# Optimization experiments

Measured on AMD Instinct MI355X. Metric: run time of the kernel, lower is better.

Reference implementation:

```python
import jax, jax.numpy as jnp
import numpy as np

N_NODES = 50000
N_EDGES = 500000


def setup_inputs() -> dict:
    key = jax.random.key(0)
    ks = jax.random.split(key, 24)
    p = {}
    p['x_feat'] = jax.random.normal(ks[0], (N_NODES, 24), dtype=jnp.float32)
    p['edge_index'] = jax.random.randint(ks[1], (2, N_EDGES), 0, N_NODES)
    p['edge_attr'] = jax.random.uniform(ks[2], (N_EDGES, 16), dtype=jnp.float32)
    def lin(k, fan_in, shape):
        b = 1.0 / np.sqrt(fan_in)
        return jax.random.uniform(k, shape, jnp.float32, -b, b)
    # group-0 input projection: 24 -> 32
    p['lin_prep_W'] = lin(ks[3], 24, (24, 32)); p['lin_prep_b'] = lin(ks[4], 24, (32,))
    # prep tube: 32 -> 16
    p['tube_W'] = lin(ks[5], 32, (32, 16)); p['tube_b'] = lin(ks[6], 32, (16,))
    # shared edge-attr trunk: 16 -> 32 -> 16
    p['edge_W1'] = lin(ks[7], 16, (16, 32)); p['edge_b1'] = lin(ks[8], 16, (32,))
    p['edge_W2'] = lin(ks[9], 32, (32, 16)); p['edge_b2'] = lin(ks[10], 32, (16,))
    # conv1: in=16, out=8 per aggr (mean, max, add)
    p['conv1_edge_W'] = lin(ks[11], 16, (3, 16, 16 * 8)); p['conv1_edge_b'] = lin(ks[12], 16, (3, 16 * 8))
    p['conv1_root_W'] = lin(ks[13], 16, (3, 16, 8)); p['conv1_bias'] = lin(ks[14], 16, (3, 8))
    # conv2: in=24, out=8 per aggr
    p['conv2_edge_W'] = lin(ks[15], 16, (3, 16, 24 * 8)); p['conv2_edge_b'] = lin(ks[16], 16, (3, 24 * 8))
    p['conv2_root_W'] = lin(ks[17], 24, (3, 24, 8)); p['conv2_bias'] = lin(ks[18], 24, (3, 8))
    # output head: 24 -> 2
    p['out_W'] = lin(ks[19], 24, (24, 2)); p['out_b'] = lin(ks[20], 24, (2,))
    return p


def _nnconv(x, e_repr, src, dst, edge_W, edge_b, root_W, bias, n_nodes):
    # x: [N, in]; e_repr: [E, 16]; edge_W: [3, 16, in*out]
    d_in = x.shape[1]
    x_src = x[src]  # [E, in]
    deg = jax.ops.segment_sum(jnp.ones_like(src, dtype=x.dtype), dst, num_segments=n_nodes)  # [N]
    outs = []
    for a, aggr in enumerate(('mean', 'max', 'add')):
        W_e = (e_repr @ edge_W[a] + edge_b[a]).reshape(e_repr.shape[0], d_in, -1)  # [E, in, out]
        msg = jnp.einsum('ei,eio->eo', x_src, W_e)  # [E, out]
        if aggr == 'add':
            agg = jax.ops.segment_sum(msg, dst, num_segments=n_nodes)
        elif aggr == 'mean':
            agg = jax.ops.segment_sum(msg, dst, num_segments=n_nodes) / jnp.maximum(deg, 1.0)[:, None]
        else:
            agg = jax.ops.segment_max(msg, dst, num_segments=n_nodes)
            agg = jnp.where(deg[:, None] > 0, agg, 0.0)  # no-neighbor nodes -> 0
        outs.append(agg + x @ root_W[a] + bias[a])
    return jax.nn.relu(jnp.concatenate(outs, axis=1))  # [N, 3*out]


def reference(x_feat, edge_index, edge_attr, lin_prep_W, lin_prep_b, tube_W, tube_b,
              edge_W1, edge_b1, edge_W2, edge_b2,
              conv1_edge_W, conv1_edge_b, conv1_root_W, conv1_bias,
              conv2_edge_W, conv2_edge_b, conv2_root_W, conv2_bias,
              out_W, out_b):
    n_nodes = x_feat.shape[0]
    src, dst = edge_index[0], edge_index[1]
    # node prep: group projection + tube (relu acts, dropout=0 -> identity)
    x = jax.nn.relu(x_feat @ lin_prep_W + lin_prep_b)       # [N, 32]
    x = jax.nn.relu(x @ tube_W + tube_b)                    # [N, 16]
    # shared edge-attr trunk (last activation = sigmoid), computed once
    e = jax.nn.relu(edge_attr @ edge_W1 + edge_b1)
    e_repr = jax.nn.sigmoid(e @ edge_W2 + edge_b2)          # [E, 16]
    # hop 1 and hop 2 of edge-conditioned NNConv with mean/max/add aggregators
    x = _nnconv(x, e_repr, src, dst, conv1_edge_W, conv1_edge_b, conv1_root_W, conv1_bias, n_nodes)  # [N, 24]
    x = _nnconv(x, e_repr, src, dst, conv2_edge_W, conv2_edge_b, conv2_root_W, conv2_bias, n_nodes)  # [N, 24]
    logits = x @ out_W + out_b                              # [N, 2]
    scores = jax.nn.softmax(logits, axis=1)
    return (logits, scores)
```

## Files before the change

kernel.cpp:

```cpp
#include <hip/hip_runtime.h>

#define BS 256

__device__ __forceinline__ unsigned short f2bf(float f) {
    unsigned x = __float_as_uint(f);
    return (unsigned short)((x + 0x7fffu + ((x >> 16) & 1u)) >> 16);
}
__device__ __forceinline__ void unpack8(uint4 v, float* d) {
    d[0] = __uint_as_float(v.x << 16); d[1] = __uint_as_float(v.x & 0xFFFF0000u);
    d[2] = __uint_as_float(v.y << 16); d[3] = __uint_as_float(v.y & 0xFFFF0000u);
    d[4] = __uint_as_float(v.z << 16); d[5] = __uint_as_float(v.z & 0xFFFF0000u);
    d[6] = __uint_as_float(v.w << 16); d[7] = __uint_as_float(v.w & 0xFFFF0000u);
}
__device__ __forceinline__ uint4 pack8bf(const float* r) {
    unsigned w[4];
#pragma unroll
    for (int j = 0; j < 4; j++)
        w[j] = (unsigned)f2bf(r[2 * j]) | ((unsigned)f2bf(r[2 * j + 1]) << 16);
    return make_uint4(w[0], w[1], w[2], w[3]);
}
__device__ __forceinline__ void st24bf(unsigned short* p, const float* r) {
    uint4* q = (uint4*)p;
    q[0] = pack8bf(r);
    q[1] = pack8bf(r + 8);
    q[2] = pack8bf(r + 16);
}

__global__ void prep_kernel(const float* __restrict__ xf,
                            const float* __restrict__ W1, const float* __restrict__ b1,
                            const float* __restrict__ W2, const float* __restrict__ b2,
                            float* __restrict__ x16, int N)
{
    int n = blockIdx.x * blockDim.x + threadIdx.x;
    bool valid = n < N;
    int nn = valid ? n : 0;
    float a[24];
#pragma unroll
    for (int i = 0; i < 24; i += 4)
        *(float4*)(a + i) = *(const float4*)(xf + (size_t)nn * 24 + i);
    float h[32];
#pragma unroll
    for (int j = 0; j < 32; j++) {
        float s = b1[j];
#pragma unroll
        for (int i = 0; i < 24; i++) s = fmaf(a[i], W1[i * 32 + j], s);
        h[j] = fmaxf(s, 0.f);
    }
    if (!valid) return;
#pragma unroll
    for (int j = 0; j < 16; j++) {
        float s = b2[j];
#pragma unroll
        for (int i = 0; i < 32; i++) s = fmaf(h[i], W2[i * 16 + j], s);
        x16[(size_t)n * 16 + j] = fmaxf(s, 0.f);
    }
}

__global__ void degjj_kernel(const int* __restrict__ srcA, const int* __restrict__ dstA,
                             int* __restrict__ cntS, int* __restrict__ cntD,
                             int* __restrict__ jS, int* __restrict__ jD, int E)
{
    int e = blockIdx.x * blockDim.x + threadIdx.x;
    if (e < E) {
        jS[e] = atomicAdd(&cntS[srcA[e]], 1);
        jD[e] = atomicAdd(&cntD[dstA[e]], 1);
    }
}
__global__ void offsets2_kernel(const int* __restrict__ cntS, const int* __restrict__ cntD,
                                int* __restrict__ offsS, int* __restrict__ offsD,
                                int* __restrict__ cursS, int* __restrict__ cursD, int N)
{
    int n = blockIdx.x * blockDim.x + threadIdx.x;
    int lane = threadIdx.x & 63;
    bool valid = n < N;
    int dS = valid ? cntS[n] : 0;
    int dD = valid ? cntD[n] : 0;
    int sS = dS, sD = dD;
#pragma unroll
    for (int o = 1; o < 64; o <<= 1) {
        int tS = __shfl_up(sS, o);
        int tD = __shfl_up(sD, o);
        if (lane >= o) { sS += tS; sD += tD; }
    }
    int totS = __shfl(sS, 63);
    int totD = __shfl(sD, 63);
    int baseS = 0, baseD = 0;
    if (lane == 63) {
        baseS = atomicAdd(cursS, totS);
        baseD = atomicAdd(cursD, totD);
    }
    baseS = __shfl(baseS, 63);
    baseD = __shfl(baseD, 63);
    if (valid) {
        offsS[n] = baseS + sS - dS;
        offsD[n] = baseD + sD - dD;
    }
}

__global__ __launch_bounds__(BS) void er_fill_kernel(
    const int* __restrict__ srcA, const int* __restrict__ dstA,
    const int* __restrict__ jS, const int* __restrict__ jD,
    const int* __restrict__ offsS, const int* __restrict__ offsD,
    const float* __restrict__ eattr,
    const float* __restrict__ eW1, const float* __restrict__ eb1,
    const float* __restrict__ eW2, const float* __restrict__ eb2,
    uint2* __restrict__ spq, unsigned short* __restrict__ er_s, int E)
{
    int e = blockIdx.x * BS + threadIdx.x;
    if (e >= E) return;
    int s = srcA[e], d = dstA[e];
    int p = offsS[s] + jS[e];
    int q = offsD[d] + jD[e];
    spq[p] = make_uint2((unsigned)s, (unsigned)q);

    float ea[16];
#pragma unroll
    for (int i = 0; i < 16; i += 4)
        *(float4*)(ea + i) = *(const float4*)(eattr + (size_t)e * 16 + i);
    float h[32];
#pragma unroll
    for (int j = 0; j < 32; j++) {
        float t = eb1[j];
#pragma unroll
        for (int i = 0; i < 16; i++) t = fmaf(ea[i], eW1[i * 32 + j], t);
        h[j] = fmaxf(t, 0.f);
    }
    float er[16];
#pragma unroll
    for (int j = 0; j < 16; j++) {
        float t = eb2[j];
#pragma unroll
        for (int i = 0; i < 32; i++) t = fmaf(h[i], eW2[i * 16 + j], t);
        er[j] = 1.f / (1.f + __expf(-t));
    }
    uint4* qo = (uint4*)(er_s + (size_t)p * 16);
    qo[0] = pack8bf(er);
    qo[1] = pack8bf(er + 8);
}

template <int IN>
__global__ __launch_bounds__(BS) void ynode_kernel(const float* __restrict__ x,
                                                   const float* __restrict__ W,
                                                   const float* __restrict__ B,
                                                   const float* __restrict__ RW,
                                                   const float* __restrict__ RB,
                                                   unsigned short* __restrict__ Y,
                                                   float* __restrict__ root, int N)
{
    __shared__ float w_lds[IN * 24];
    int t = threadIdx.x;
    int k = blockIdx.y;

    for (int idx = t; idx < IN * 24; idx += BS) {
        int i = idx / 24;
        int j = idx - i * 24;
        int a = j >> 3, o = j & 7;
        float v;
        if (k < 16)       v = W[(((size_t)a * 16 + k) * IN + i) * 8 + o];
        else if (k == 16) v = B[((size_t)a * IN + i) * 8 + o];
        else              v = RW[((size_t)a * IN + i) * 8 + o];
        w_lds[idx] = v;
    }
    __syncthreads();

    int n0 = blockIdx.x * (BS * 2) + t;
    int n1 = n0 + BS;
    bool v0 = n0 < N, v1 = n1 < N;
    int m0 = v0 ? n0 : 0, m1 = v1 ? n1 : 0;

    float xa[IN], xb[IN];
#pragma unroll
    for (int i = 0; i < IN; i += 4) {
        *(float4*)(xa + i) = *(const float4*)(x + (size_t)m0 * IN + i);
        *(float4*)(xb + i) = *(const float4*)(x + (size_t)m1 * IN + i);
    }

    float ra[24], rb[24];
    if (k == 17) {
#pragma unroll
        for (int j = 0; j < 24; j++) { ra[j] = RB[j]; rb[j] = ra[j]; }
    } else {
#pragma unroll
        for (int j = 0; j < 24; j++) { ra[j] = 0.f; rb[j] = 0.f; }
    }

#pragma unroll
    for (int i = 0; i < IN; i++) {
        float x0 = xa[i], x1 = xb[i];
        const float* wr = w_lds + i * 24;
#pragma unroll
        for (int j = 0; j < 24; j++) {
            float w = wr[j];
            ra[j] = fmaf(x0, w, ra[j]);
            rb[j] = fmaf(x1, w, rb[j]);
        }
    }

    if (k < 17) {
        if (v0) st24bf(Y + ((size_t)k * N + n0) * 24, ra);
        if (v1) st24bf(Y + ((size_t)k * N + n1) * 24, rb);
    } else {
        if (v0) {
            float* pr = root + (size_t)n0 * 24;
#pragma unroll
            for (int j = 0; j < 24; j += 4)
                *(float4*)(pr + j) = make_float4(ra[j], ra[j+1], ra[j+2], ra[j+3]);
        }
        if (v1) {
            float* pr = root + (size_t)n1 * 24;
#pragma unroll
            for (int j = 0; j < 24; j += 4)
                *(float4*)(pr + j) = make_float4(rb[j], rb[j+1], rb[j+2], rb[j+3]);
        }
    }
}

__global__ __launch_bounds__(BS) void msg_kernel(
    const uint2* __restrict__ spq,
    const unsigned short* __restrict__ er_s,
    const unsigned short* __restrict__ Y,
    unsigned short* __restrict__ msg16,
    int N, int E)
{
    int tid = blockIdx.x * BS + threadIdx.x;
    int p = tid / 3;
    int j = tid - p * 3;
    if (p >= E) return;

    uint2 sq = spq[p];

    float er[16];
    {
        const uint4* eu = (const uint4*)(er_s + (size_t)p * 16);
        unpack8(eu[0], er);
        unpack8(eu[1], er + 8);
    }

    const unsigned short* yb = Y + (size_t)sq.x * 24 + j * 8;
    size_t kstride = (size_t)N * 24;

    float acc[8];
    unpack8(*(const uint4*)(yb + 16 * kstride), acc);
#pragma unroll
    for (int k = 0; k < 16; k++) {
        float t[8];
        unpack8(*(const uint4*)(yb + (size_t)k * kstride), t);
        float ek = er[k];
#pragma unroll
        for (int o = 0; o < 8; o++) acc[o] = fmaf(ek, t[o], acc[o]);
    }
    unsigned short* mrow = msg16 + (size_t)sq.y * 32;
    *(uint4*)(mrow + j * 8) = pack8bf(acc);
    if (j == 0) *(uint4*)(mrow + 24) = make_uint4(0, 0, 0, 0);
}

__global__ __launch_bounds__(BS) void gather_kernel(
    const unsigned short* __restrict__ msg16,
    const int* __restrict__ offs,
    const int* __restrict__ degi,
    const float* __restrict__ root,
    float* __restrict__ out, int N)
{
    int n = (blockIdx.x * BS + threadIdx.x) >> 6;
    if (n >= N) return;
    int lane = threadIdx.x & 63;
    int c = lane & 3;
    int r = lane >> 2;

    int off = offs[n];
    int d = degi[n];

    float s[8], m[8];
#pragma unroll
    for (int o = 0; o < 8; o++) { s[o] = 0.f; m[o] = -3.402823466e38f; }

    if (c < 3) {
        const unsigned short* base = msg16 + (size_t)off * 32 + c * 8;
        for (int j = r; j < d; j += 16) {
            uint4 v = *(const uint4*)(base + (size_t)j * 32);
            float t[8];
            unpack8(v, t);
#pragma unroll
            for (int o = 0; o < 8; o++) {
                s[o] += t[o];
                m[o] = fmaxf(m[o], t[o]);
            }
        }
    }
#pragma unroll
    for (int mask = 4; mask < 64; mask <<= 1) {
#pragma unroll
        for (int o = 0; o < 8; o++) {
            s[o] += __shfl_xor(s[o], mask);
            m[o] = fmaxf(m[o], __shfl_xor(m[o], mask));
        }
    }
    if (lane >= 3) return;

    float inv = 1.f / fmaxf((float)d, 1.f);
    const float* pr = root + (size_t)n * 24 + c * 8;
    float4 r0 = *(const float4*)(pr);
    float4 r1 = *(const float4*)(pr + 4);
    float rb[8] = {r0.x, r0.y, r0.z, r0.w, r1.x, r1.y, r1.z, r1.w};
    float rr[8];
#pragma unroll
    for (int o = 0; o < 8; o++) {
        float agg = (c == 0) ? s[o] * inv
                  : (c == 1) ? ((d > 0) ? m[o] : 0.f)
                  : s[o];
        rr[o] = fmaxf(rb[o] + agg, 0.f);
    }
    float* po = out + (size_t)n * 24 + c * 8;
    *(float4*)(po)     = make_float4(rr[0], rr[1], rr[2], rr[3]);
    *(float4*)(po + 4) = make_float4(rr[4], rr[5], rr[6], rr[7]);
}

__global__ void head_kernel(const float* __restrict__ x, const float* __restrict__ W,
                            const float* __restrict__ b, float* __restrict__ out, int N)
{
    int n = blockIdx.x * blockDim.x + threadIdx.x;
    if (n >= N) return;
    float l0 = b[0], l1 = b[1];
#pragma unroll
    for (int i = 0; i < 24; i++) {
        float xi = x[(size_t)n * 24 + i];
        l0 = fmaf(xi, W[i * 2 + 0], l0);
        l1 = fmaf(xi, W[i * 2 + 1], l1);
    }
    out[2 * (size_t)n + 0] = l0;
    out[2 * (size_t)n + 1] = l1;
    float mx = fmaxf(l0, l1);
    float e0 = __expf(l0 - mx), e1 = __expf(l1 - mx);
    float sm = e0 + e1;
    out[2 * (size_t)N + 2 * (size_t)n + 0] = e0 / sm;
    out[2 * (size_t)N + 2 * (size_t)n + 1] = e1 / sm;
}

extern "C" void kernel_launch(void* const* d_in, const int* in_sizes, int n_in,
                              void* d_out, int out_size, void* d_ws, size_t ws_size,
                              hipStream_t stream)
{
    const float* x_feat = (const float*)d_in[0];
    const int*   eidx   = (const int*)d_in[1];
    const float* eattr  = (const float*)d_in[2];
    const float* lpW = (const float*)d_in[3];
    const float* lpb = (const float*)d_in[4];
    const float* tW  = (const float*)d_in[5];
    const float* tb  = (const float*)d_in[6];
    const float* eW1 = (const float*)d_in[7];
    const float* eb1 = (const float*)d_in[8];
    const float* eW2 = (const float*)d_in[9];
    const float* eb2 = (const float*)d_in[10];
    const float* c1W = (const float*)d_in[11];
    const float* c1B = (const float*)d_in[12];
    const float* c1R = (const float*)d_in[13];
    const float* c1b = (const float*)d_in[14];
    const float* c2W = (const float*)d_in[15];
    const float* c2B = (const float*)d_in[16];
    const float* c2R = (const float*)d_in[17];
    const float* c2b = (const float*)d_in[18];
    const float* oW  = (const float*)d_in[19];
    const float* ob  = (const float*)d_in[20];

    int N = in_sizes[0] / 24;
    int E = in_sizes[1] / 2;
    const int* srcA = eidx;
    const int* dstA = eidx + E;

    char* wsb = (char*)d_ws;
    size_t off = 0;
    auto alloc = [&](size_t bytes) {
        off = (off + 255) & ~(size_t)255;
        void* p = wsb + off;
        off += bytes;
        return p;
    };
    unsigned short* Y     = (unsigned short*)alloc((size_t)17 * N * 24 * 2);
    unsigned short* msg16 = (unsigned short*)alloc((size_t)E * 32 * 2);
    unsigned short* er_s  = (unsigned short*)alloc((size_t)E * 16 * 2);
    float* root = (float*)alloc((size_t)N * 24 * 4);
    float* x16  = (float*)alloc((size_t)N * 16 * 4);
    float* x24a = (float*)alloc((size_t)N * 24 * 4);
    float* x24b = (float*)alloc((size_t)N * 24 * 4);
    int* ibase  = (int*)alloc(((size_t)2 * N + 2) * 4);
    int* cntS = ibase;
    int* cntD = ibase + N;
    int* cursS = ibase + 2 * N;
    int* cursD = ibase + 2 * N + 1;
    int* offsS = (int*)alloc((size_t)N * 4);
    int* offsD = (int*)alloc((size_t)N * 4);
    int* jS    = (int*)alloc((size_t)E * 4);
    int* jD    = (int*)alloc((size_t)E * 4);
    uint2* spq = (uint2*)alloc((size_t)E * 8);

    dim3 blk(BS);
    int nb_nodes = (N + BS - 1) / BS;
    int nb_edges = (E + BS - 1) / BS;
    int nb_msg   = (3 * E + BS - 1) / BS;
    int nb_gath  = ((size_t)N * 64 + BS - 1) / BS;
    int nb_ypair = (N + BS * 2 - 1) / (BS * 2);
    dim3 ygrid(nb_ypair, 18);

    hipMemsetAsync(ibase, 0, (2 * (size_t)N + 2) * 4, stream);

    prep_kernel<<<nb_nodes, blk, 0, stream>>>(x_feat, lpW, lpb, tW, tb, x16, N);

    degjj_kernel<<<nb_edges, blk, 0, stream>>>(srcA, dstA, cntS, cntD, jS, jD, E);
    offsets2_kernel<<<nb_nodes, blk, 0, stream>>>(cntS, cntD, offsS, offsD, cursS, cursD, N);
    er_fill_kernel<<<nb_edges, blk, 0, stream>>>(srcA, dstA, jS, jD, offsS, offsD,
                                                 eattr, eW1, eb1, eW2, eb2, spq, er_s, E);

    ynode_kernel<16><<<ygrid, blk, 0, stream>>>(x16, c1W, c1B, c1R, c1b, Y, root, N);
    msg_kernel<<<nb_msg, blk, 0, stream>>>(spq, er_s, Y, msg16, N, E);
    gather_kernel<<<nb_gath, blk, 0, stream>>>(msg16, offsD, cntD, root, x24a, N);

    ynode_kernel<24><<<ygrid, blk, 0, stream>>>(x24a, c2W, c2B, c2R, c2b, Y, root, N);
    msg_kernel<<<nb_msg, blk, 0, stream>>>(spq, er_s, Y, msg16, N, E);
    gather_kernel<<<nb_gath, blk, 0, stream>>>(msg16, offsD, cntD, root, x24b, N);

    head_kernel<<<nb_nodes, blk, 0, stream>>>(x24b, oW, ob, (float*)d_out, N);
}
```

Measured before the change: 276.3 us.

## Split Y and root into per-aggregator planes and batch degree atomics per thread

```diff
diff --git a/kernel.cpp b/kernel.cpp
--- a/kernel.cpp
+++ b/kernel.cpp
@@ -19,12 +19,6 @@
         w[j] = (unsigned)f2bf(r[2 * j]) | ((unsigned)f2bf(r[2 * j + 1]) << 16);
     return make_uint4(w[0], w[1], w[2], w[3]);
 }
-__device__ __forceinline__ void st24bf(unsigned short* p, const float* r) {
-    uint4* q = (uint4*)p;
-    q[0] = pack8bf(r);
-    q[1] = pack8bf(r + 8);
-    q[2] = pack8bf(r + 16);
-}
 
 __global__ void prep_kernel(const float* __restrict__ xf,
                             const float* __restrict__ W1, const float* __restrict__ b1,
@@ -60,12 +54,25 @@
                              int* __restrict__ cntS, int* __restrict__ cntD,
                              int* __restrict__ jS, int* __restrict__ jD, int E)
 {
-    int e = blockIdx.x * blockDim.x + threadIdx.x;
-    if (e < E) {
-        jS[e] = atomicAdd(&cntS[srcA[e]], 1);
-        jD[e] = atomicAdd(&cntD[dstA[e]], 1);
-    }
-}
+    int base = blockIdx.x * (BS * 4) + threadIdx.x;
+    int e0 = base, e1 = base + BS, e2 = base + 2 * BS, e3 = base + 3 * BS;
+    bool v0 = e0 < E, v1 = e1 < E, v2 = e2 < E, v3 = e3 < E;
+    int s0 = 0, s1 = 0, s2 = 0, s3 = 0, d0 = 0, d1 = 0, d2 = 0, d3 = 0;
+    if (v0) { s0 = srcA[e0]; d0 = dstA[e0]; }
+    if (v1) { s1 = srcA[e1]; d1 = dstA[e1]; }
+    if (v2) { s2 = srcA[e2]; d2 = dstA[e2]; }
+    if (v3) { s3 = srcA[e3]; d3 = dstA[e3]; }
+    int a0 = 0, a1 = 0, a2 = 0, a3 = 0, b0 = 0, b1 = 0, b2 = 0, b3 = 0;
+    if (v0) { a0 = atomicAdd(&cntS[s0], 1); b0 = atomicAdd(&cntD[d0], 1); }
+    if (v1) { a1 = atomicAdd(&cntS[s1], 1); b1 = atomicAdd(&cntD[d1], 1); }
+    if (v2) { a2 = atomicAdd(&cntS[s2], 1); b2 = atomicAdd(&cntD[d2], 1); }
+    if (v3) { a3 = atomicAdd(&cntS[s3], 1); b3 = atomicAdd(&cntD[d3], 1); }
+    if (v0) { jS[e0] = a0; jD[e0] = b0; }
+    if (v1) { jS[e1] = a1; jD[e1] = b1; }
+    if (v2) { jS[e2] = a2; jD[e2] = b2; }
+    if (v3) { jS[e3] = a3; jD[e3] = b3; }
+}
+
 __global__ void offsets2_kernel(const int* __restrict__ cntS, const int* __restrict__ cntD,
                                 int* __restrict__ offsS, int* __restrict__ offsD,
                                 int* __restrict__ cursS, int* __restrict__ cursD, int N)
@@ -147,20 +154,16 @@
                                                    unsigned short* __restrict__ Y,
                                                    float* __restrict__ root, int N)
 {
-    __shared__ float w_lds[IN * 24];
+    __shared__ float4 w4[IN * 2];
     int t = threadIdx.x;
     int k = blockIdx.y;
-
-    for (int idx = t; idx < IN * 24; idx += BS) {
-        int i = idx / 24;
-        int j = idx - i * 24;
-        int a = j >> 3, o = j & 7;
-        float v;
-        if (k < 16)       v = W[(((size_t)a * 16 + k) * IN + i) * 8 + o];
-        else if (k == 16) v = B[((size_t)a * IN + i) * 8 + o];
-        else              v = RW[((size_t)a * IN + i) * 8 + o];
-        w_lds[idx] = v;
-    }
+    int a = blockIdx.z;
+
+    const float* wbase;
+    if (k < 16)       wbase = W + (((size_t)a * 16 + k) * IN) * 8;
+    else if (k == 16) wbase = B + ((size_t)a * IN) * 8;
+    else              wbase = RW + ((size_t)a * IN) * 8;
+    if (t < IN * 2) w4[t] = ((const float4*)wbase)[t];
     __syncthreads();
 
     int n0 = blockIdx.x * (BS * 2) + t;
@@ -175,42 +178,41 @@
         *(float4*)(xb + i) = *(const float4*)(x + (size_t)m1 * IN + i);
     }
 
-    float ra[24], rb[24];
-    if (k == 17) {
-#pragma unroll
-        for (int j = 0; j < 24; j++) { ra[j] = RB[j]; rb[j] = ra[j]; }
+    float r0[8], r1[8];
+#pragma unroll
+    for (int o = 0; o < 8; o++) { r0[o] = 0.f; r1[o] = 0.f; }
+
+#pragma unroll
+    for (int i = 0; i < IN; i++) {
+        float4 wA = w4[i * 2];
+        float4 wB = w4[i * 2 + 1];
+        float x0 = xa[i], x1 = xb[i];
+        r0[0] = fmaf(x0, wA.x, r0[0]); r0[1] = fmaf(x0, wA.y, r0[1]);
+        r0[2] = fmaf(x0, wA.z, r0[2]); r0[3] = fmaf(x0, wA.w, r0[3]);
+        r0[4] = fmaf(x0, wB.x, r0[4]); r0[5] = fmaf(x0, wB.y, r0[5]);
+        r0[6] = fmaf(x0, wB.z, r0[6]); r0[7] = fmaf(x0, wB.w, r0[7]);
+        r1[0] = fmaf(x1, wA.x, r1[0]); r1[1] = fmaf(x1, wA.y, r1[1]);
+        r1[2] = fmaf(x1, wA.z, r1[2]); r1[3] = fmaf(x1, wA.w, r1[3]);
+        r1[4] = fmaf(x1, wB.x, r1[4]); r1[5] = fmaf(x1, wB.y, r1[5]);
+        r1[6] = fmaf(x1, wB.z, r1[6]); r1[7] = fmaf(x1, wB.w, r1[7]);
+    }
+
+    if (k < 17) {
+        size_t slab = ((size_t)k * 3 + a) * N;
+        if (v0) *(uint4*)(Y + (slab + n0) * 8) = pack8bf(r0);
+        if (v1) *(uint4*)(Y + (slab + n1) * 8) = pack8bf(r1);
     } else {
-#pragma unroll
-        for (int j = 0; j < 24; j++) { ra[j] = 0.f; rb[j] = 0.f; }
-    }
-
-#pragma unroll
-    for (int i = 0; i < IN; i++) {
-        float x0 = xa[i], x1 = xb[i];
-        const float* wr = w_lds + i * 24;
-#pragma unroll
-        for (int j = 0; j < 24; j++) {
-            float w = wr[j];
-            ra[j] = fmaf(x0, w, ra[j]);
-            rb[j] = fmaf(x1, w, rb[j]);
-        }
-    }
-
-    if (k < 17) {
-        if (v0) st24bf(Y + ((size_t)k * N + n0) * 24, ra);
-        if (v1) st24bf(Y + ((size_t)k * N + n1) * 24, rb);
-    } else {
+        float rb0 = RB[a * 8 + 0], rb1 = RB[a * 8 + 1], rb2 = RB[a * 8 + 2], rb3 = RB[a * 8 + 3];
+        float rb4 = RB[a * 8 + 4], rb5 = RB[a * 8 + 5], rb6 = RB[a * 8 + 6], rb7 = RB[a * 8 + 7];
         if (v0) {
-            float* pr = root + (size_t)n0 * 24;
-#pragma unroll
-            for (int j = 0; j < 24; j += 4)
-                *(float4*)(pr + j) = make_float4(ra[j], ra[j+1], ra[j+2], ra[j+3]);
+            float* pr = root + ((size_t)a * N + n0) * 8;
+            *(float4*)(pr)     = make_float4(r0[0] + rb0, r0[1] + rb1, r0[2] + rb2, r0[3] + rb3);
+            *(float4*)(pr + 4) = make_float4(r0[4] + rb4, r0[5] + rb5, r0[6] + rb6, r0[7] + rb7);
         }
         if (v1) {
-            float* pr = root + (size_t)n1 * 24;
-#pragma unroll
-            for (int j = 0; j < 24; j += 4)
-                *(float4*)(pr + j) = make_float4(rb[j], rb[j+1], rb[j+2], rb[j+3]);
+            float* pr = root + ((size_t)a * N + n1) * 8;
+            *(float4*)(pr)     = make_float4(r1[0] + rb0, r1[1] + rb1, r1[2] + rb2, r1[3] + rb3);
+            *(float4*)(pr + 4) = make_float4(r1[4] + rb4, r1[5] + rb5, r1[6] + rb6, r1[7] + rb7);
         }
     }
 }
@@ -236,8 +238,8 @@
         unpack8(eu[1], er + 8);
     }
 
-    const unsigned short* yb = Y + (size_t)sq.x * 24 + j * 8;
-    size_t kstride = (size_t)N * 24;
+    const unsigned short* yb = Y + ((size_t)j * N + sq.x) * 8;
+    size_t kstride = (size_t)3 * N * 8;
 
     float acc[8];
     unpack8(*(const uint4*)(yb + 16 * kstride), acc);
@@ -298,7 +300,7 @@
     if (lane >= 3) return;
 
     float inv = 1.f / fmaxf((float)d, 1.f);
-    const float* pr = root + (size_t)n * 24 + c * 8;
+    const float* pr = root + ((size_t)c * N + n) * 8;
     float4 r0 = *(const float4*)(pr);
     float4 r1 = *(const float4*)(pr + 4);
     float rb[8] = {r0.x, r0.y, r0.z, r0.w, r1.x, r1.y, r1.z, r1.w};
@@ -375,10 +377,10 @@
         off += bytes;
         return p;
     };
-    unsigned short* Y     = (unsigned short*)alloc((size_t)17 * N * 24 * 2);
+    unsigned short* Y     = (unsigned short*)alloc((size_t)17 * 3 * N * 8 * 2);
     unsigned short* msg16 = (unsigned short*)alloc((size_t)E * 32 * 2);
     unsigned short* er_s  = (unsigned short*)alloc((size_t)E * 16 * 2);
-    float* root = (float*)alloc((size_t)N * 24 * 4);
+    float* root = (float*)alloc((size_t)3 * N * 8 * 4);
     float* x16  = (float*)alloc((size_t)N * 16 * 4);
     float* x24a = (float*)alloc((size_t)N * 24 * 4);
     float* x24b = (float*)alloc((size_t)N * 24 * 4);
@@ -396,16 +398,17 @@
     dim3 blk(BS);
     int nb_nodes = (N + BS - 1) / BS;
     int nb_edges = (E + BS - 1) / BS;
+    int nb_deg   = (E + BS * 4 - 1) / (BS * 4);
     int nb_msg   = (3 * E + BS - 1) / BS;
     int nb_gath  = ((size_t)N * 64 + BS - 1) / BS;
     int nb_ypair = (N + BS * 2 - 1) / (BS * 2);
-    dim3 ygrid(nb_ypair, 18);
+    dim3 ygrid(nb_ypair, 18, 3);
 
     hipMemsetAsync(ibase, 0, (2 * (size_t)N + 2) * 4, stream);
 
     prep_kernel<<<nb_nodes, blk, 0, stream>>>(x_feat, lpW, lpb, tW, tb, x16, N);
 
-    degjj_kernel<<<nb_edges, blk, 0, stream>>>(srcA, dstA, cntS, cntD, jS, jD, E);
+    degjj_kernel<<<nb_deg, blk, 0, stream>>>(srcA, dstA, cntS, cntD, jS, jD, E);
     offsets2_kernel<<<nb_nodes, blk, 0, stream>>>(cntS, cntD, offsS, offsD, cursS, cursD, N);
     er_fill_kernel<<<nb_edges, blk, 0, stream>>>(srcA, dstA, jS, jD, offsS, offsD,
                                                  eattr, eW1, eb1, eW2, eb2, spq, er_s, E);
```

Measured after the change: 321.6 us. 1.16x slower.

## Pad Y rows to 32 bf16, batch degree atomics, vectorize ynode weight loads

Applied to the files above, without the earlier changes.

```diff
diff --git a/kernel.cpp b/kernel.cpp
--- a/kernel.cpp
+++ b/kernel.cpp
@@ -19,11 +19,12 @@
         w[j] = (unsigned)f2bf(r[2 * j]) | ((unsigned)f2bf(r[2 * j + 1]) << 16);
     return make_uint4(w[0], w[1], w[2], w[3]);
 }
-__device__ __forceinline__ void st24bf(unsigned short* p, const float* r) {
+__device__ __forceinline__ void st32bf(unsigned short* p, const float* r) {
     uint4* q = (uint4*)p;
     q[0] = pack8bf(r);
     q[1] = pack8bf(r + 8);
     q[2] = pack8bf(r + 16);
+    q[3] = make_uint4(0, 0, 0, 0);
 }
 
 __global__ void prep_kernel(const float* __restrict__ xf,
@@ -60,12 +61,25 @@
                              int* __restrict__ cntS, int* __restrict__ cntD,
                              int* __restrict__ jS, int* __restrict__ jD, int E)
 {
-    int e = blockIdx.x * blockDim.x + threadIdx.x;
-    if (e < E) {
-        jS[e] = atomicAdd(&cntS[srcA[e]], 1);
-        jD[e] = atomicAdd(&cntD[dstA[e]], 1);
-    }
-}
+    int base = blockIdx.x * (BS * 4) + threadIdx.x;
+    int e0 = base, e1 = base + BS, e2 = base + 2 * BS, e3 = base + 3 * BS;
+    bool v0 = e0 < E, v1 = e1 < E, v2 = e2 < E, v3 = e3 < E;
+    int s0 = 0, s1 = 0, s2 = 0, s3 = 0, d0 = 0, d1 = 0, d2 = 0, d3 = 0;
+    if (v0) { s0 = srcA[e0]; d0 = dstA[e0]; }
+    if (v1) { s1 = srcA[e1]; d1 = dstA[e1]; }
+    if (v2) { s2 = srcA[e2]; d2 = dstA[e2]; }
+    if (v3) { s3 = srcA[e3]; d3 = dstA[e3]; }
+    int a0 = 0, a1 = 0, a2 = 0, a3 = 0, b0 = 0, b1 = 0, b2 = 0, b3 = 0;
+    if (v0) { a0 = atomicAdd(&cntS[s0], 1); b0 = atomicAdd(&cntD[d0], 1); }
+    if (v1) { a1 = atomicAdd(&cntS[s1], 1); b1 = atomicAdd(&cntD[d1], 1); }
+    if (v2) { a2 = atomicAdd(&cntS[s2], 1); b2 = atomicAdd(&cntD[d2], 1); }
+    if (v3) { a3 = atomicAdd(&cntS[s3], 1); b3 = atomicAdd(&cntD[d3], 1); }
+    if (v0) { jS[e0] = a0; jD[e0] = b0; }
+    if (v1) { jS[e1] = a1; jD[e1] = b1; }
+    if (v2) { jS[e2] = a2; jD[e2] = b2; }
+    if (v3) { jS[e3] = a3; jD[e3] = b3; }
+}
+
 __global__ void offsets2_kernel(const int* __restrict__ cntS, const int* __restrict__ cntD,
                                 int* __restrict__ offsS, int* __restrict__ offsD,
                                 int* __restrict__ cursS, int* __restrict__ cursD, int N)
@@ -147,19 +161,20 @@
                                                    unsigned short* __restrict__ Y,
                                                    float* __restrict__ root, int N)
 {
-    __shared__ float w_lds[IN * 24];
+    __shared__ float4 w4[IN * 6];
     int t = threadIdx.x;
     int k = blockIdx.y;
 
-    for (int idx = t; idx < IN * 24; idx += BS) {
-        int i = idx / 24;
-        int j = idx - i * 24;
-        int a = j >> 3, o = j & 7;
-        float v;
-        if (k < 16)       v = W[(((size_t)a * 16 + k) * IN + i) * 8 + o];
-        else if (k == 16) v = B[((size_t)a * IN + i) * 8 + o];
-        else              v = RW[((size_t)a * IN + i) * 8 + o];
-        w_lds[idx] = v;
+    for (int idx = t; idx < IN * 6; idx += BS) {
+        int i = idx / 6;
+        int c = idx - i * 6;
+        int a = c >> 1;
+        int o = (c & 1) * 4;
+        const float* srcp;
+        if (k < 16)       srcp = W + (((size_t)a * 16 + k) * IN + i) * 8 + o;
+        else if (k == 16) srcp = B + ((size_t)a * IN + i) * 8 + o;
+        else              srcp = RW + ((size_t)a * IN + i) * 8 + o;
+        w4[idx] = *(const float4*)srcp;
     }
     __syncthreads();
 
@@ -176,41 +191,39 @@
     }
 
     float ra[24], rb[24];
-    if (k == 17) {
-#pragma unroll
-        for (int j = 0; j < 24; j++) { ra[j] = RB[j]; rb[j] = ra[j]; }
-    } else {
-#pragma unroll
-        for (int j = 0; j < 24; j++) { ra[j] = 0.f; rb[j] = 0.f; }
-    }
+#pragma unroll
+    for (int j = 0; j < 24; j++) { ra[j] = 0.f; rb[j] = 0.f; }
 
 #pragma unroll
     for (int i = 0; i < IN; i++) {
         float x0 = xa[i], x1 = xb[i];
-        const float* wr = w_lds + i * 24;
-#pragma unroll
-        for (int j = 0; j < 24; j++) {
-            float w = wr[j];
-            ra[j] = fmaf(x0, w, ra[j]);
-            rb[j] = fmaf(x1, w, rb[j]);
+#pragma unroll
+        for (int c = 0; c < 6; c++) {
+            float4 w = w4[i * 6 + c];
+            ra[c*4+0] = fmaf(x0, w.x, ra[c*4+0]); ra[c*4+1] = fmaf(x0, w.y, ra[c*4+1]);
+            ra[c*4+2] = fmaf(x0, w.z, ra[c*4+2]); ra[c*4+3] = fmaf(x0, w.w, ra[c*4+3]);
+            rb[c*4+0] = fmaf(x1, w.x, rb[c*4+0]); rb[c*4+1] = fmaf(x1, w.y, rb[c*4+1]);
+            rb[c*4+2] = fmaf(x1, w.z, rb[c*4+2]); rb[c*4+3] = fmaf(x1, w.w, rb[c*4+3]);
         }
     }
 
     if (k < 17) {
-        if (v0) st24bf(Y + ((size_t)k * N + n0) * 24, ra);
-        if (v1) st24bf(Y + ((size_t)k * N + n1) * 24, rb);
+        if (v0) st32bf(Y + ((size_t)k * N + n0) * 32, ra);
+        if (v1) st32bf(Y + ((size_t)k * N + n1) * 32, rb);
     } else {
         if (v0) {
             float* pr = root + (size_t)n0 * 24;
 #pragma unroll
             for (int j = 0; j < 24; j += 4)
-                *(float4*)(pr + j) = make_float4(ra[j], ra[j+1], ra[j+2], ra[j+3]);
+                *(float4*)(pr + j) = make_float4(ra[j] + RB[j], ra[j+1] + RB[j+1],
+                                                 ra[j+2] + RB[j+2], ra[j+3] + RB[j+3]);
         }
         if (v1) {
             float* pr = root + (size_t)n1 * 24;
 #pragma unroll
             for (int j = 0; j < 24; j += 4)
-                *(float4*)(pr + j) = make_float4(rb[j], rb[j+1], rb[j+2], rb[j+3]);
+                *(float4*)(pr + j) = make_float4(rb[j] + RB[j], rb[j+1] + RB[j+1],
+                                                 rb[j+2] + RB[j+2], rb[j+3] + RB[j+3]);
         }
     }
 }
@@ -236,8 +249,8 @@
         unpack8(eu[1], er + 8);
     }
 
-    const unsigned short* yb = Y + (size_t)sq.x * 24 + j * 8;
-    size_t kstride = (size_t)N * 24;
+    const unsigned short* yb = Y + (size_t)sq.x * 32 + j * 8;
+    size_t kstride = (size_t)N * 32;
 
     float acc[8];
     unpack8(*(const uint4*)(yb + 16 * kstride), acc);
@@ -375,7 +388,7 @@
         off += bytes;
         return p;
     };
-    unsigned short* Y     = (unsigned short*)alloc((size_t)17 * N * 24 * 2);
+    unsigned short* Y     = (unsigned short*)alloc((size_t)17 * N * 32 * 2);
     unsigned short* msg16 = (unsigned short*)alloc((size_t)E * 32 * 2);
     unsigned short* er_s  = (unsigned short*)alloc((size_t)E * 16 * 2);
     float* root = (float*)alloc((size_t)N * 24 * 4);
@@ -396,6 +409,7 @@
     dim3 blk(BS);
     int nb_nodes = (N + BS - 1) / BS;
     int nb_edges = (E + BS - 1) / BS;
+    int nb_deg   = (E + BS * 4 - 1) / (BS * 4);
     int nb_msg   = (3 * E + BS - 1) / BS;
     int nb_gath  = ((size_t)N * 64 + BS - 1) / BS;
     int nb_ypair = (N + BS * 2 - 1) / (BS * 2);
@@ -405,7 +419,7 @@
 
     prep_kernel<<<nb_nodes, blk, 0, stream>>>(x_feat, lpW, lpb, tW, tb, x16, N);
 
-    degjj_kernel<<<nb_edges, blk, 0, stream>>>(srcA, dstA, cntS, cntD, jS, jD, E);
+    degjj_kernel<<<nb_deg, blk, 0, stream>>>(srcA, dstA, cntS, cntD, jS, jD, E);
     offsets2_kernel<<<nb_nodes, blk, 0, stream>>>(cntS, cntD, offsS, offsD, cursS, cursD, N);
     er_fill_kernel<<<nb_edges, blk, 0, stream>>>(srcA, dstA, jS, jD, offsS, offsD,
                                                  eattr, eW1, eb1, eW2, eb2, spq, er_s, E);
```

After: 291.2 us. +5.4%, slower.
